# Performance work log

Measured on AMD Instinct MI355X. Metric: run time of the kernel, lower is better.

## Reference

```python
import jax, jax.numpy as jnp
import numpy as np
from jax import lax

B, N, S, C_IN, C_OUT = 4, 16384, 4096, 256, 256


def setup_inputs() -> dict:
    key = jax.random.key(0)
    k1, k2, k3, k4 = jax.random.split(key, 4)
    xyz1 = jax.random.normal(k1, (B, 3, N), dtype=jnp.float32)
    xyz2 = jax.random.normal(k2, (B, 3, S), dtype=jnp.float32)
    points2 = jax.random.normal(k3, (B, C_IN, S), dtype=jnp.float32)
    W = jax.random.normal(k4, (C_OUT, C_IN), dtype=jnp.float32) * (1.0 / np.sqrt(C_IN))
    b = jnp.zeros((C_OUT,), dtype=jnp.float32)
    return {"xyz1": xyz1, "xyz2": xyz2, "points2": points2, "W": W, "b": b}


def reference(xyz1, xyz2, points2, W, b):
    # channel-first -> channel-last
    p1 = jnp.transpose(xyz1, (0, 2, 1))        # [B, N, 3]
    p2 = jnp.transpose(xyz2, (0, 2, 1))        # [B, S, 3]
    f2 = jnp.transpose(points2, (0, 2, 1))     # [B, S, C]
    Bn, Nn, _ = p1.shape
    Cn = f2.shape[-1]
    # squared pairwise distances [B, N, S]
    d = (-2.0 * jnp.einsum('bnc,bsc->bns', p1, p2)
         + jnp.sum(p1 * p1, axis=-1)[:, :, None]
         + jnp.sum(p2 * p2, axis=-1)[:, None, :])
    # 3 nearest neighbors (smallest distances) -- equivalent to sort + slice :3
    neg_d3, idx = lax.top_k(-d, 3)             # [B, N, 3]
    d3 = -neg_d3
    recip = 1.0 / (d3 + 1e-8)
    weight = recip / jnp.sum(recip, axis=-1, keepdims=True)   # [B, N, 3]
    # gather neighbor features: [B, N, 3, C]
    gathered = jnp.take_along_axis(
        f2, idx.reshape(Bn, Nn * 3)[..., None], axis=1
    ).reshape(Bn, Nn, 3, Cn)
    interp = jnp.sum(gathered * weight[..., None], axis=2)    # [B, N, C]
    # Conv1d(kernel=1) == per-point linear: [B, C_out, N]
    out = jnp.einsum('bnc,oc->bon', interp, W) + b[None, :, None]
    return out
```

## Files before the change

### kernel.cpp

```cpp
#include <hip/hip_runtime.h>

#define BB 4
#define NN 16384
#define SS 4096
#define CIN 256
#define COUT 256

#define SC 8
#define SCS (SS / SC)
#define FUSEB 1024

typedef float v2f __attribute__((ext_vector_type(2)));
typedef float v4f __attribute__((ext_vector_type(4)));

__device__ __forceinline__ unsigned short f2bf(float f) {
    unsigned u = __float_as_uint(f);
    u += 0x7FFF + ((u >> 16) & 1);
    return (unsigned short)(u >> 16);
}
__device__ __forceinline__ float bf2f(unsigned short h) {
    return __uint_as_float((unsigned)h << 16);
}

__device__ __forceinline__ double pack_key(float e, unsigned gs) {
    double kd = (double)e + 640.0;
    unsigned long long b = __double_as_longlong(kd);
    b = (b & 0xFFFFFFFFFFFFF000ULL) | (unsigned long long)gs;
    return __longlong_as_double((long long)b);
}
__device__ __forceinline__ void insert_key(double& k0, double& k1, double& k2,
                                           double x) {
    double m  = fmax(k0, x);
    k0 = fmin(k0, x);
    double m2 = fmax(k1, m);
    k1 = fmin(k1, m);
    k2 = fmin(k2, m2);
}

#define PK_LO(acc, ap, bw)                                                     \
    asm("v_pk_fma_f32 %0, %1, %2, %0 op_sel:[0,0,0] op_sel_hi:[0,1,1]"         \
        : "+v"(acc) : "v"(ap), "v"(bw))
#define PK_HI(acc, ap, bw)                                                     \
    asm("v_pk_fma_f32 %0, %1, %2, %0 op_sel:[1,0,0] op_sel_hi:[1,1,1]"         \
        : "+v"(acc) : "v"(ap), "v"(bw))

__device__ __forceinline__ void knn_phase(int bid, int t, float* smem,
                                          const float* __restrict__ xyz1,
                                          const float* __restrict__ xyz2,
                                          unsigned long long* __restrict__ pk) {
    int nb = bid & 31;
    int ch = (bid >> 5) & 7;
    int b  = bid >> 8;
    int s0 = ch * SCS;

    float4* smv = (float4*)smem;
    const float* x2 = xyz2 + (size_t)b * 3 * SS;
    __syncthreads();
    for (int i = t; i < SCS; i += 256) {
        float px = x2[s0 + i];
        float py = x2[SS + s0 + i];
        float pz = x2[2 * SS + s0 + i];
        smv[i] = make_float4(px, py, pz, fmaf(px, px, fmaf(py, py, pz * pz)));
    }
    __syncthreads();

    int n0  = nb * 512 + t;
    int n1q = n0 + 256;
    const float* xb = xyz1 + (size_t)b * 3 * NN;
    float ax = xb[n0],  ay = xb[NN + n0],  az = xb[2 * NN + n0];
    float bx = xb[n1q], by = xb[NN + n1q], bz = xb[2 * NN + n1q];
    v2f XX = {-2.0f * ax, -2.0f * bx};
    v2f YY = {-2.0f * ay, -2.0f * by};
    v2f ZZ = {-2.0f * az, -2.0f * bz};

    double AK0 = 1023.0, AK1 = 1023.0, AK2 = 1023.0;
    double BK0 = 1023.0, BK1 = 1023.0, BK2 = 1023.0;

#pragma unroll 8
    for (int s = 0; s < SCS; ++s) {
        v4f p = *(const v4f*)(smem + 4 * s);
        v2f pxy = __builtin_shufflevector(p, p, 0, 1);
        v2f pzw = __builtin_shufflevector(p, p, 2, 3);
        v2f e2;
        asm("v_pk_fma_f32 %0, %1, %2, %3 op_sel:[0,0,1] op_sel_hi:[0,1,1]"
            : "=v"(e2) : "v"(pzw), "v"(ZZ), "v"(pzw));
        asm("v_pk_fma_f32 %0, %1, %2, %0 op_sel:[1,0,0] op_sel_hi:[1,1,1]"
            : "+v"(e2) : "v"(pxy), "v"(YY));
        asm("v_pk_fma_f32 %0, %1, %2, %0 op_sel:[0,0,0] op_sel_hi:[0,1,1]"
            : "+v"(e2) : "v"(pxy), "v"(XX));
        unsigned gs = (unsigned)(s0 + s);
        insert_key(AK0, AK1, AK2, pack_key(e2.x, gs));
        insert_key(BK0, BK1, BK2, pack_key(e2.y, gs));
    }

    size_t cb = (size_t)(ch * BB + b) * 3;
    pk[(cb + 0) * NN + n0]  = (unsigned long long)__double_as_longlong(AK0);
    pk[(cb + 1) * NN + n0]  = (unsigned long long)__double_as_longlong(AK1);
    pk[(cb + 2) * NN + n0]  = (unsigned long long)__double_as_longlong(AK2);
    pk[(cb + 0) * NN + n1q] = (unsigned long long)__double_as_longlong(BK0);
    pk[(cb + 1) * NN + n1q] = (unsigned long long)__double_as_longlong(BK1);
    pk[(cb + 2) * NN + n1q] = (unsigned long long)__double_as_longlong(BK2);
}

__device__ __forceinline__ void gemm_phase(int bid, int t, float* smem,
                                           const float* __restrict__ P,
                                           const float* __restrict__ W,
                                           const float* __restrict__ bias,
                                           unsigned short* __restrict__ Gh) {
    int o0 = (bid & 3) * 64;
    int s0 = ((bid >> 2) & 63) * 64;
    int b  = bid >> 8;
    float* sP = smem;
    float* sW = smem + 1024;
    int i = t & 15;
    int j = t >> 4;

    v2f acc2[4][2];
#pragma unroll
    for (int p = 0; p < 4; ++p) {
        acc2[p][0] = (v2f){0.f, 0.f};
        acc2[p][1] = (v2f){0.f, 0.f};
    }

    const float* Pb = P + (size_t)b * CIN * SS;

    for (int c0 = 0; c0 < CIN; c0 += 16) {
        __syncthreads();
        {
            int col = t & 63;
            int r0r = t >> 6;
#pragma unroll
            for (int r = 0; r < 4; ++r) {
                int row = r0r + r * 4;
                sP[row * 64 + col] = Pb[(size_t)(c0 + row) * SS + s0 + col];
            }
        }
        {
            int cc = t & 15;
            int obase = t >> 4;
#pragma unroll
            for (int r = 0; r < 4; ++r) {
                int oo = obase + 16 * r;
                sW[cc * 68 + oo] = W[(size_t)(o0 + oo) * CIN + c0 + cc];
            }
        }
        __syncthreads();

#pragma unroll
        for (int cc = 0; cc < 16; ++cc) {
            v4f a  = *(const v4f*)&sP[cc * 64 + i * 4];
            v4f bv = *(const v4f*)&sW[cc * 68 + j * 4];
            v2f a01 = __builtin_shufflevector(a, a, 0, 1);
            v2f a23 = __builtin_shufflevector(a, a, 2, 3);
            v2f b01 = __builtin_shufflevector(bv, bv, 0, 1);
            v2f b23 = __builtin_shufflevector(bv, bv, 2, 3);
            PK_LO(acc2[0][0], a01, b01); PK_LO(acc2[0][1], a01, b23);
            PK_HI(acc2[1][0], a01, b01); PK_HI(acc2[1][1], a01, b23);
            PK_LO(acc2[2][0], a23, b01); PK_LO(acc2[2][1], a23, b23);
            PK_HI(acc2[3][0], a23, b01); PK_HI(acc2[3][1], a23, b23);
        }
    }

    float b0 = bias[o0 + j * 4 + 0];
    float b1 = bias[o0 + j * 4 + 1];
    float b2 = bias[o0 + j * 4 + 2];
    float b3 = bias[o0 + j * 4 + 3];
#pragma unroll
    for (int p = 0; p < 4; ++p) {
        ushort4 v;
        v.x = f2bf(acc2[p][0].x + b0);
        v.y = f2bf(acc2[p][0].y + b1);
        v.z = f2bf(acc2[p][1].x + b2);
        v.w = f2bf(acc2[p][1].y + b3);
        size_t off = ((size_t)b * SS + s0 + i * 4 + p) * COUT + o0 + j * 4;
        *(ushort4*)&Gh[off] = v;
    }
}

__global__ __launch_bounds__(256) void k_fused(const float* __restrict__ xyz1,
                                               const float* __restrict__ xyz2,
                                               const float* __restrict__ P,
                                               const float* __restrict__ W,
                                               const float* __restrict__ bias,
                                               unsigned short* __restrict__ Gh,
                                               unsigned long long* __restrict__ pk) {
    __shared__ float smem[2112];
    int bid = blockIdx.x;
    int t   = threadIdx.x;

    if (((bid >> 8) & 1) == 0) {
        knn_phase(bid, t, smem, xyz1, xyz2, pk);
        gemm_phase(bid, t, smem, P, W, bias, Gh);
    } else {
        gemm_phase(bid, t, smem, P, W, bias, Gh);
        knn_phase(bid, t, smem, xyz1, xyz2, pk);
    }
}

__global__ __launch_bounds__(256) void k_merge(const unsigned long long* __restrict__ pk,
                                               const float* __restrict__ xyz1,
                                               float4* __restrict__ wi4,
                                               int4* __restrict__ gi4) {
    int b = blockIdx.y;
    int n = blockIdx.x * 256 + threadIdx.x;

    double k0 = 1023.0, k1 = 1023.0, k2 = 1023.0;
#pragma unroll
    for (int ch = 0; ch < SC; ++ch) {
        size_t cb = (size_t)(ch * BB + b) * 3;
#pragma unroll
        for (int j = 0; j < 3; ++j) {
            double x = __longlong_as_double(
                (long long)pk[(cb + j) * NN + n]);
            insert_key(k0, k1, k2, x);
        }
    }

    const float* xb = xyz1 + (size_t)b * 3 * NN;
    float qx = xb[n], qy = xb[NN + n], qz = xb[2 * NN + n];
    float n1 = fmaf(qx, qx, fmaf(qy, qy, qz * qz));

    unsigned long long u0 = (unsigned long long)__double_as_longlong(k0);
    unsigned long long u1 = (unsigned long long)__double_as_longlong(k1);
    unsigned long long u2 = (unsigned long long)__double_as_longlong(k2);
    float e0 = (float)(__longlong_as_double((long long)(u0 & ~0xFFFULL)) - 640.0);
    float e1 = (float)(__longlong_as_double((long long)(u1 & ~0xFFFULL)) - 640.0);
    float e2 = (float)(__longlong_as_double((long long)(u2 & ~0xFFFULL)) - 640.0);
    float d0 = e0 + n1, d1 = e1 + n1, d2 = e2 + n1;

    float r0 = 1.0f / (d0 + 1e-8f);
    float r1 = 1.0f / (d1 + 1e-8f);
    float r2 = 1.0f / (d2 + 1e-8f);
    float inv = 1.0f / (r0 + r1 + r2);
    size_t q = (size_t)b * NN + n;
    wi4[q] = make_float4(r0 * inv, r1 * inv, r2 * inv, 0.f);
    gi4[q] = make_int4((int)(u0 & 0xFFFULL), (int)(u1 & 0xFFFULL),
                       (int)(u2 & 0xFFFULL), 0);
}

__global__ __launch_bounds__(256) void k_out(const unsigned short* __restrict__ Gh,
                                             const float4* __restrict__ wi4,
                                             const int4* __restrict__ gi4,
                                             float* __restrict__ out) {
    __shared__ float  tile[64 * 68];
    __shared__ float4 swv[64];
    __shared__ int4   siv[64];
    int bid  = blockIdx.x;
    int x    = bid & 7;
    int b    = x >> 1;
    int local = (bid >> 3) + (x & 1) * 512;
    int nb   = local & 255;
    int oc   = local >> 8;
    int n0   = nb * 64;
    int o0   = oc * 64;
    int t    = threadIdx.x;
    int wave = t >> 6;
    int lane = t & 63;
    int qg   = lane >> 4;
    int c16  = lane & 15;

    if (t < 64) {
        size_t q = (size_t)b * NN + n0 + t;
        swv[t] = wi4[q];
        siv[t] = gi4[q];
    }
    __syncthreads();

    const unsigned short* Gb = Gh + (size_t)b * SS * COUT;

#pragma unroll
    for (int pass = 0; pass < 4; ++pass) {
        int q = pass * 16 + wave * 4 + qg;
        float4 wv = swv[q];
        int4   iv = siv[q];
        int co = o0 + c16 * 4;
        ushort4 a0 = *(const ushort4*)(Gb + (size_t)iv.x * COUT + co);
        ushort4 a1 = *(const ushort4*)(Gb + (size_t)iv.y * COUT + co);
        ushort4 a2 = *(const ushort4*)(Gb + (size_t)iv.z * COUT + co);
        float4 v;
        v.x = fmaf(wv.x, bf2f(a0.x), fmaf(wv.y, bf2f(a1.x), wv.z * bf2f(a2.x)));
        v.y = fmaf(wv.x, bf2f(a0.y), fmaf(wv.y, bf2f(a1.y), wv.z * bf2f(a2.y)));
        v.z = fmaf(wv.x, bf2f(a0.z), fmaf(wv.y, bf2f(a1.z), wv.z * bf2f(a2.z)));
        v.w = fmaf(wv.x, bf2f(a0.w), fmaf(wv.y, bf2f(a1.w), wv.z * bf2f(a2.w)));
        *(float4*)&tile[q * 68 + c16 * 4] = v;
    }
    __syncthreads();

    float* obase = out + ((size_t)b * COUT + o0) * NN + n0 + lane;
#pragma unroll
    for (int g = 0; g < 4; ++g) {
        int c = wave * 16 + g * 4;
        float4 v = *(const float4*)&tile[lane * 68 + c];
        obase[(size_t)(c + 0) * NN] = v.x;
        obase[(size_t)(c + 1) * NN] = v.y;
        obase[(size_t)(c + 2) * NN] = v.z;
        obase[(size_t)(c + 3) * NN] = v.w;
    }
}

extern "C" void kernel_launch(void* const* d_in, const int* in_sizes, int n_in,
                              void* d_out, int out_size, void* d_ws, size_t ws_size,
                              hipStream_t stream) {
    const float* xyz1    = (const float*)d_in[0];
    const float* xyz2    = (const float*)d_in[1];
    const float* points2 = (const float*)d_in[2];
    const float* W       = (const float*)d_in[3];
    const float* bias    = (const float*)d_in[4];
    float* out = (float*)d_out;

    char* ws = (char*)d_ws;
    unsigned long long* pk  = (unsigned long long*)(ws);
    unsigned short*     Gh  = (unsigned short*)(ws + 12582912);
    float4*             wi4 = (float4*)(ws + 20971520);
    int4*               gi4 = (int4*)(ws + 22020096);

    k_fused<<<dim3(FUSEB), 256, 0, stream>>>(xyz1, xyz2, points2, W, bias,
                                             Gh, pk);
    k_merge<<<dim3(NN / 256, BB), 256, 0, stream>>>(pk, xyz1, wi4, gi4);
    k_out<<<dim3(4096), 256, 0, stream>>>(Gh, wi4, gi4, out);
}
```

Measured before the change: 214.7 us.

## Two-pass float threshold KNN with halved S-chunks and split KNN/GEMM blocks

The KNN phase now runs a cheap first pass that tracks the three smallest float distances using fmed3. A second pass builds packed double keys only for candidates at or below the third-smallest threshold, and skips wavefronts where no lane qualifies. The S dimension is split into 4 chunks instead of 8, which halves the partial-result buffer and the work in the merge step. The fused kernel now interleaves separate KNN and GEMM blocks (one in three) instead of running both phases in every block. The distance computation is done twice, and each block gets larger LDS and longer per-block work.

```diff
diff --git a/kernel.cpp b/kernel.cpp
--- a/kernel.cpp
+++ b/kernel.cpp
@@ -6,9 +6,10 @@
 #define CIN 256
 #define COUT 256
 
-#define SC 8
+#define SC 4
 #define SCS (SS / SC)
-#define FUSEB 1024
+#define KNNB ((NN / 512) * SC * BB)
+#define GEMMB ((COUT / 64) * (SS / 64) * BB)
 
 typedef float v2f __attribute__((ext_vector_type(2)));
 typedef float v4f __attribute__((ext_vector_type(4)));
@@ -37,6 +38,16 @@
     k2 = fmin(k2, m2);
 }
 
+#define E2_FROM(p_xy, p_zw, XX, YY, ZZ, e2)                                    \
+    do {                                                                       \
+        asm("v_pk_fma_f32 %0, %1, %2, %3 op_sel:[0,0,1] op_sel_hi:[0,1,1]"     \
+            : "=v"(e2) : "v"(p_zw), "v"(ZZ), "v"(p_zw));                       \
+        asm("v_pk_fma_f32 %0, %1, %2, %0 op_sel:[1,0,0] op_sel_hi:[1,1,1]"     \
+            : "+v"(e2) : "v"(p_xy), "v"(YY));                                  \
+        asm("v_pk_fma_f32 %0, %1, %2, %0 op_sel:[0,0,0] op_sel_hi:[0,1,1]"     \
+            : "+v"(e2) : "v"(p_xy), "v"(XX));                                  \
+    } while (0)
+
 #define PK_LO(acc, ap, bw)                                                     \
     asm("v_pk_fma_f32 %0, %1, %2, %0 op_sel:[0,0,0] op_sel_hi:[0,1,1]"         \
         : "+v"(acc) : "v"(ap), "v"(bw))
@@ -44,18 +55,17 @@
     asm("v_pk_fma_f32 %0, %1, %2, %0 op_sel:[1,0,0] op_sel_hi:[1,1,1]"         \
         : "+v"(acc) : "v"(ap), "v"(bw))
 
-__device__ __forceinline__ void knn_phase(int bid, int t, float* smem,
+__device__ __forceinline__ void knn_phase(int id, int t, float* smem,
                                           const float* __restrict__ xyz1,
                                           const float* __restrict__ xyz2,
                                           unsigned long long* __restrict__ pk) {
-    int nb = bid & 31;
-    int ch = (bid >> 5) & 7;
-    int b  = bid >> 8;
+    int nb = id & 31;
+    int ch = (id >> 5) & (SC - 1);
+    int b  = id >> 7;
     int s0 = ch * SCS;
 
     float4* smv = (float4*)smem;
     const float* x2 = xyz2 + (size_t)b * 3 * SS;
-    __syncthreads();
     for (int i = t; i < SCS; i += 256) {
         float px = x2[s0 + i];
         float py = x2[SS + s0 + i];
@@ -73,43 +83,60 @@
     v2f YY = {-2.0f * ay, -2.0f * by};
     v2f ZZ = {-2.0f * az, -2.0f * bz};
 
-    double AK0 = 1023.0, AK1 = 1023.0, AK2 = 1023.0;
-    double BK0 = 1023.0, BK1 = 1023.0, BK2 = 1023.0;
-
+    float mA0 = 1e30f, mA1 = 1e30f, mA2 = 1e30f;
+    float mB0 = 1e30f, mB1 = 1e30f, mB2 = 1e30f;
 #pragma unroll 8
     for (int s = 0; s < SCS; ++s) {
         v4f p = *(const v4f*)(smem + 4 * s);
         v2f pxy = __builtin_shufflevector(p, p, 0, 1);
         v2f pzw = __builtin_shufflevector(p, p, 2, 3);
         v2f e2;
-        asm("v_pk_fma_f32 %0, %1, %2, %3 op_sel:[0,0,1] op_sel_hi:[0,1,1]"
-            : "=v"(e2) : "v"(pzw), "v"(ZZ), "v"(pzw));
-        asm("v_pk_fma_f32 %0, %1, %2, %0 op_sel:[1,0,0] op_sel_hi:[1,1,1]"
-            : "+v"(e2) : "v"(pxy), "v"(YY));
-        asm("v_pk_fma_f32 %0, %1, %2, %0 op_sel:[0,0,0] op_sel_hi:[0,1,1]"
-            : "+v"(e2) : "v"(pxy), "v"(XX));
-        unsigned gs = (unsigned)(s0 + s);
-        insert_key(AK0, AK1, AK2, pack_key(e2.x, gs));
-        insert_key(BK0, BK1, BK2, pack_key(e2.y, gs));
-    }
-
-    size_t cb = (size_t)(ch * BB + b) * 3;
-    pk[(cb + 0) * NN + n0]  = (unsigned long long)__double_as_longlong(AK0);
-    pk[(cb + 1) * NN + n0]  = (unsigned long long)__double_as_longlong(AK1);
-    pk[(cb + 2) * NN + n0]  = (unsigned long long)__double_as_longlong(AK2);
-    pk[(cb + 0) * NN + n1q] = (unsigned long long)__double_as_longlong(BK0);
-    pk[(cb + 1) * NN + n1q] = (unsigned long long)__double_as_longlong(BK1);
-    pk[(cb + 2) * NN + n1q] = (unsigned long long)__double_as_longlong(BK2);
-}
-
-__device__ __forceinline__ void gemm_phase(int bid, int t, float* smem,
+        E2_FROM(pxy, pzw, XX, YY, ZZ, e2);
+        float nA1 = __builtin_amdgcn_fmed3f(e2.x, mA0, mA1);
+        float nA2 = __builtin_amdgcn_fmed3f(e2.x, mA1, mA2);
+        mA0 = fminf(mA0, e2.x);
+        mA1 = nA1; mA2 = nA2;
+        float nB1 = __builtin_amdgcn_fmed3f(e2.y, mB0, mB1);
+        float nB2 = __builtin_amdgcn_fmed3f(e2.y, mB1, mB2);
+        mB0 = fminf(mB0, e2.y);
+        mB1 = nB1; mB2 = nB2;
+    }
+
+    double AK0 = 1023.0, AK1 = 1023.0, AK2 = 1023.0;
+    double BK0 = 1023.0, BK1 = 1023.0, BK2 = 1023.0;
+#pragma unroll 4
+    for (int s = 0; s < SCS; ++s) {
+        v4f p = *(const v4f*)(smem + 4 * s);
+        v2f pxy = __builtin_shufflevector(p, p, 0, 1);
+        v2f pzw = __builtin_shufflevector(p, p, 2, 3);
+        v2f e2;
+        E2_FROM(pxy, pzw, XX, YY, ZZ, e2);
+        bool ca = (e2.x <= mA2);
+        bool cb = (e2.y <= mB2);
+        if (__any(ca || cb)) {
+            unsigned gs = (unsigned)(s0 + s);
+            if (ca) insert_key(AK0, AK1, AK2, pack_key(e2.x, gs));
+            if (cb) insert_key(BK0, BK1, BK2, pack_key(e2.y, gs));
+        }
+    }
+
+    size_t cbk = (size_t)(ch * BB + b) * 3;
+    pk[(cbk + 0) * NN + n0]  = (unsigned long long)__double_as_longlong(AK0);
+    pk[(cbk + 1) * NN + n0]  = (unsigned long long)__double_as_longlong(AK1);
+    pk[(cbk + 2) * NN + n0]  = (unsigned long long)__double_as_longlong(AK2);
+    pk[(cbk + 0) * NN + n1q] = (unsigned long long)__double_as_longlong(BK0);
+    pk[(cbk + 1) * NN + n1q] = (unsigned long long)__double_as_longlong(BK1);
+    pk[(cbk + 2) * NN + n1q] = (unsigned long long)__double_as_longlong(BK2);
+}
+
+__device__ __forceinline__ void gemm_phase(int g, int t, float* smem,
                                            const float* __restrict__ P,
                                            const float* __restrict__ W,
                                            const float* __restrict__ bias,
                                            unsigned short* __restrict__ Gh) {
-    int o0 = (bid & 3) * 64;
-    int s0 = ((bid >> 2) & 63) * 64;
-    int b  = bid >> 8;
+    int o0 = (g & 3) * 64;
+    int s0 = ((g >> 2) & 63) * 64;
+    int b  = g >> 8;
     float* sP = smem;
     float* sW = smem + 1024;
     int i = t & 15;
@@ -184,16 +211,14 @@
                                                const float* __restrict__ bias,
                                                unsigned short* __restrict__ Gh,
                                                unsigned long long* __restrict__ pk) {
-    __shared__ float smem[2112];
+    __shared__ float smem[4096];
     int bid = blockIdx.x;
     int t   = threadIdx.x;
 
-    if (((bid >> 8) & 1) == 0) {
-        knn_phase(bid, t, smem, xyz1, xyz2, pk);
-        gemm_phase(bid, t, smem, P, W, bias, Gh);
+    if (bid % 3 == 0) {
+        knn_phase(bid / 3, t, smem, xyz1, xyz2, pk);
     } else {
-        gemm_phase(bid, t, smem, P, W, bias, Gh);
-        knn_phase(bid, t, smem, xyz1, xyz2, pk);
+        gemm_phase(bid - bid / 3 - 1, t, smem, P, W, bias, Gh);
     }
 }
 
@@ -310,12 +335,12 @@
 
     char* ws = (char*)d_ws;
     unsigned long long* pk  = (unsigned long long*)(ws);
-    unsigned short*     Gh  = (unsigned short*)(ws + 12582912);
-    float4*             wi4 = (float4*)(ws + 20971520);
-    int4*               gi4 = (int4*)(ws + 22020096);
-
-    k_fused<<<dim3(FUSEB), 256, 0, stream>>>(xyz1, xyz2, points2, W, bias,
-                                             Gh, pk);
+    unsigned short*     Gh  = (unsigned short*)(ws + 6291456);
+    float4*             wi4 = (float4*)(ws + 14680064);
+    int4*               gi4 = (int4*)(ws + 15728640);
+
+    k_fused<<<dim3(KNNB + GEMMB), 256, 0, stream>>>(xyz1, xyz2, points2, W, bias,
+                                                    Gh, pk);
     k_merge<<<dim3(NN / 256, BB), 256, 0, stream>>>(pk, xyz1, wi4, gi4);
     k_out<<<dim3(4096), 256, 0, stream>>>(Gh, wi4, gi4, out);
 }
```

Result: slower. 266.4 us (+24.1%).
